# Kernel optimization log

Hardware: AMD Instinct MI355X
Metric: run time of the kernel (lower is better)

## Reference

```python
import jax, jax.numpy as jnp
import numpy as np

N_HEADS = 32
N_KV_HEADS = 8


def _rope_tables(T, half_dim):
    # standard rotary angle tables: theta_i = 10000^(-2i/D)
    inv_freq = 1.0 / (10000.0 ** (np.arange(half_dim, dtype=np.float32) / half_dim))
    ang = np.arange(T, dtype=np.float32)[:, None] * inv_freq[None, :]  # [T, D/2]
    return jnp.asarray(np.sin(ang)), jnp.asarray(np.cos(ang))


def setup_inputs() -> dict:
    key = jax.random.key(0)
    ks = jax.random.split(key, 5)
    B, T, C = 1, 2048, 2048
    hd = C // N_HEADS  # 64
    kv_dim = N_KV_HEADS * hd  # 512
    w_scale = 0.02
    x = jax.random.normal(ks[0], (B, T, C), dtype=jnp.float32)
    Wq = jax.random.normal(ks[1], (C, C), dtype=jnp.float32) * w_scale
    Wk = jax.random.normal(ks[2], (C, kv_dim), dtype=jnp.float32) * w_scale
    Wv = jax.random.normal(ks[3], (C, kv_dim), dtype=jnp.float32) * w_scale
    Wo = jax.random.normal(ks[4], (C, C), dtype=jnp.float32) * w_scale
    rope_sin, rope_cos = _rope_tables(T, hd // 2)
    return {"x": x, "Wq": Wq, "Wk": Wk, "Wv": Wv, "Wo": Wo,
            "rope_sin": rope_sin, "rope_cos": rope_cos, "swa_window": 1024}


def apply_rope(x, sin, cos):
    # x: [B, T, H, D]; sin/cos: [T, D/2]; interleaved-pair rotation
    B, T, H, D = x.shape
    xr = x.reshape(B, T, H, D // 2, 2)
    x1, x2 = xr[..., 0], xr[..., 1]
    s = sin[None, :, None, :]
    c = cos[None, :, None, :]
    o1 = x1 * c - x2 * s
    o2 = x1 * s + x2 * c
    return jnp.stack((o1, o2), axis=-1).reshape(B, T, H, D)


def reference(x, Wq, Wk, Wv, Wo, rope_sin, rope_cos, swa_window):
    B, T, C = x.shape
    hd = C // N_HEADS
    g = N_HEADS // N_KV_HEADS
    q = (x @ Wq).reshape(B, T, N_HEADS, hd)
    k = (x @ Wk).reshape(B, T, N_KV_HEADS, hd)
    v = (x @ Wv).reshape(B, T, N_KV_HEADS, hd)
    q = apply_rope(q, rope_sin, rope_cos)
    k = apply_rope(k, rope_sin, rope_cos)
    # GQA: expand kv heads (repeat_interleave along head dim)
    k = jnp.repeat(k, g, axis=2)
    v = jnp.repeat(v, g, axis=2)
    q = q.transpose(0, 2, 1, 3)  # [B, H, T, D]
    k = k.transpose(0, 2, 1, 3)
    v = v.transpose(0, 2, 1, 3)
    scores = jnp.einsum('bhqd,bhkd->bhqk', q, k) / jnp.sqrt(jnp.float32(hd))
    idx = jnp.arange(T)
    rel = idx[:, None] - idx[None, :]  # query_pos - key_pos
    # masked-out: future tokens (rel < 0) or older than the sliding window
    masked = (rel < 0) | (rel > swa_window)
    scores = jnp.where(masked[None, None], jnp.float32(-1e30), scores)
    attn = jax.nn.softmax(scores, axis=-1)
    out = jnp.einsum('bhqk,bhkd->bhqd', attn, v)
    out = out.transpose(0, 2, 1, 3).reshape(B, T, C)
    return out @ Wo
```

## Files before the change

kernel.cpp:

```cpp
#include <hip/hip_runtime.h>

typedef __attribute__((ext_vector_type(8))) short short8;
typedef __attribute__((ext_vector_type(4))) float f32x4;
typedef unsigned short u16;

#define T_SEQ 2048
#define C_DIM 2048
#define QKV_N 3072
#define HD 64


static __device__ __forceinline__ u16 f2bf(float f) {
    unsigned u = __builtin_bit_cast(unsigned, f);
    unsigned rounding = 0x7fffu + ((u >> 16) & 1u);
    return (u16)((u + rounding) >> 16);
}

static __device__ __forceinline__ void gld_lds16(void* lds, const void* g) {
    __builtin_amdgcn_global_load_lds(
        (const __attribute__((address_space(1))) unsigned int*)g,
        (__attribute__((address_space(3))) unsigned int*)lds, 16, 0, 0);
}


__global__ __launch_bounds__(256) void convert_bf16_k(const float* __restrict__ in,
                                                      u16* __restrict__ out) {
    int i = (blockIdx.x * 256 + threadIdx.x) * 4;
    f32x4 v = *(const f32x4*)(in + i);
    u16* o = out + i;
    o[0] = f2bf(v[0]); o[1] = f2bf(v[1]); o[2] = f2bf(v[2]); o[3] = f2bf(v[3]);
}


__global__ __launch_bounds__(256) void transpose_conv(const float* __restrict__ W,
                                                      u16* __restrict__ Wt,
                                                      int N, int row_off) {
    __shared__ float tile[32][33];
    int n0 = blockIdx.x * 32, k0 = blockIdx.y * 32;
    int tx = threadIdx.x & 31, ty = threadIdx.x >> 5;
#pragma unroll
    for (int i = 0; i < 4; i++)
        tile[ty + i * 8][tx] = W[(size_t)(k0 + ty + i * 8) * N + n0 + tx];
    __syncthreads();
#pragma unroll
    for (int i = 0; i < 4; i++)
        Wt[(size_t)(row_off + n0 + ty + i * 8) * 2048 + k0 + tx] = f2bf(tile[tx][ty + i * 8]);
}


__global__ __launch_bounds__(256) void gemm_bt(const u16* __restrict__ A,
                                               const u16* __restrict__ BT,
                                               float* __restrict__ C,
                                               int M, int N, int K) {
    __shared__ alignas(16) u16 As[128][32];
    __shared__ alignas(16) u16 Bs[128][32];
    const int m0 = blockIdx.x * 128;
    const int n0 = blockIdx.y * 128;
    const int w = threadIdx.x >> 6, lane = threadIdx.x & 63;
    const int lo = lane & 15, hi = lane >> 4;
    const int wr = w >> 1, wc = w & 1;

    f32x4 zero4 = {0.f, 0.f, 0.f, 0.f};
    f32x4 acc[4][4];
#pragma unroll
    for (int m = 0; m < 4; m++)
#pragma unroll
        for (int n = 0; n < 4; n++) acc[m][n] = zero4;

    for (int k0 = 0; k0 < K; k0 += 32) {
#pragma unroll
        for (int i = 0; i < 2; i++) {
            int c = (w * 2 + i) * 64 + lane;
            int row = c >> 2, cc = (c & 3) * 8;
            gld_lds16((char*)&As[0][0] + (w * 2 + i) * 1024,
                      A + (size_t)(m0 + row) * K + k0 + cc);
            gld_lds16((char*)&Bs[0][0] + (w * 2 + i) * 1024,
                      BT + (size_t)(n0 + row) * K + k0 + cc);
        }
        __syncthreads();
        short8 a[4], b[4];
#pragma unroll
        for (int m = 0; m < 4; m++) a[m] = *(const short8*)&As[wr * 64 + m * 16 + lo][hi * 8];
#pragma unroll
        for (int n = 0; n < 4; n++) b[n] = *(const short8*)&Bs[wc * 64 + n * 16 + lo][hi * 8];
#pragma unroll
        for (int m = 0; m < 4; m++)
#pragma unroll
            for (int n = 0; n < 4; n++)
                acc[m][n] = __builtin_amdgcn_mfma_f32_16x16x32_bf16(a[m], b[n], acc[m][n], 0, 0, 0);
        __syncthreads();
    }
#pragma unroll
    for (int m = 0; m < 4; m++)
#pragma unroll
        for (int n = 0; n < 4; n++) {
            int col = n0 + wc * 64 + n * 16 + lo;
#pragma unroll
            for (int r = 0; r < 4; r++) {
                int row = m0 + wr * 64 + m * 16 + hi * 4 + r;
                C[(size_t)row * N + col] = acc[m][n][r];
            }
        }
}


__global__ __launch_bounds__(256) void rope_conv(const float* __restrict__ qkv,
                                                 const float* __restrict__ sn,
                                                 const float* __restrict__ cs,
                                                 u16* __restrict__ qb,
                                                 u16* __restrict__ kb,
                                                 u16* __restrict__ vt) {
    int t = blockIdx.x / 6;
    int idx = (blockIdx.x % 6) * 256 + threadIdx.x;
    const float* row = qkv + (size_t)t * QKV_N;
    if (idx < 1024) {
        int h = idx >> 5, pr = idx & 31;
        float x1 = row[h * 64 + 2 * pr], x2 = row[h * 64 + 2 * pr + 1];
        float s = sn[t * 32 + pr], c = cs[t * 32 + pr];
        float o1 = (x1 * c - x2 * s) * 0.125f;
        float o2 = (x1 * s + x2 * c) * 0.125f;
        unsigned pack = (unsigned)f2bf(o1) | ((unsigned)f2bf(o2) << 16);
        *(unsigned*)(qb + (size_t)t * C_DIM + h * 64 + 2 * pr) = pack;
    } else if (idx < 1280) {
        int j = idx - 1024;
        int kh = j >> 5, pr = j & 31;
        float x1 = row[2048 + kh * 64 + 2 * pr], x2 = row[2048 + kh * 64 + 2 * pr + 1];
        float s = sn[t * 32 + pr], c = cs[t * 32 + pr];
        float o1 = x1 * c - x2 * s;
        float o2 = x1 * s + x2 * c;
        unsigned pack = (unsigned)f2bf(o1) | ((unsigned)f2bf(o2) << 16);
        *(unsigned*)(kb + ((size_t)kh * T_SEQ + t) * 64 + 2 * pr) = pack;
    } else {
        int j = idx - 1280;
        int kh = j >> 5, dl = (j & 31) * 2;
        float v0 = row[2560 + kh * 64 + dl], v1 = row[2560 + kh * 64 + dl + 1];
        vt[((size_t)kh * 64 + dl) * T_SEQ + t] = f2bf(v0);
        vt[((size_t)kh * 64 + dl + 1) * T_SEQ + t] = f2bf(v1);
    }
}


__global__ __launch_bounds__(256) void attn_fwd(const u16* __restrict__ qb,
                                                const u16* __restrict__ kb,
                                                const u16* __restrict__ vt,
                                                u16* __restrict__ ob,
                                                const int* __restrict__ winp) {
    __shared__ alignas(16) char KsB[8192];
    __shared__ alignas(16) char VsB[8192];
    __shared__ alignas(16) u16 Ps[4][16][88];
    const int window = *winp;
    const int h = blockIdx.y, kvh = h >> 2;
    const int q0 = blockIdx.x * 64;
    const int w = threadIdx.x >> 6, lane = threadIdx.x & 63;
    const int lo = lane & 15, hi = lane >> 4;

    const int qrow = q0 + w * 16 + lo;
    const short8 qa0 = *(const short8*)(qb + (size_t)qrow * C_DIM + h * HD + hi * 8);
    const short8 qa1 = *(const short8*)(qb + (size_t)qrow * C_DIM + h * HD + 32 + hi * 8);

    f32x4 zero4 = {0.f, 0.f, 0.f, 0.f};
    f32x4 acc[4];
#pragma unroll
    for (int dt = 0; dt < 4; dt++) acc[dt] = zero4;
    float lreg[4] = {0.f, 0.f, 0.f, 0.f};

    int kt0 = q0 - window; if (kt0 < 0) kt0 = 0; kt0 &= ~63;
    const int qlo_w = q0 + w * 16, qhi_w = qlo_w + 15;

    for (int kt = kt0; kt < q0 + 64; kt += 64) {
#pragma unroll
        for (int j = 0; j < 2; j++) {
            int c = (w * 2 + j) * 64 + lane;
            int rr = c >> 3, sc = (c & 7) ^ (rr & 7);
            gld_lds16(KsB + (w * 2 + j) * 1024,
                      kb + ((size_t)kvh * T_SEQ + kt + rr) * 64 + sc * 8);
            gld_lds16(VsB + (w * 2 + j) * 1024,
                      vt + ((size_t)kvh * 64 + rr) * T_SEQ + kt + sc * 8);
        }
        __syncthreads();
        if (kt <= qhi_w && kt + 63 >= qlo_w - window) {
            const bool interior = (kt + 63 <= qlo_w) && (qhi_w - kt <= window);
            f32x4 s0, s1, s2, s3;
            {
#define QK_TILE(SD, NT)                                                              \
                {                                                                    \
                    int key = (NT) * 16 + lo;                                        \
                    const short8 kf0 = *(const short8*)(KsB + key * 128 + ((hi ^ (key & 7)) << 4));       \
                    const short8 kf1 = *(const short8*)(KsB + key * 128 + (((4 + hi) ^ (key & 7)) << 4)); \
                    f32x4 z = zero4;                                                 \
                    z = __builtin_amdgcn_mfma_f32_16x16x32_bf16(qa0, kf0, z, 0, 0, 0);\
                    z = __builtin_amdgcn_mfma_f32_16x16x32_bf16(qa1, kf1, z, 0, 0, 0);\
                    SD = z;                                                          \
                }
                QK_TILE(s0, 0) QK_TILE(s1, 1) QK_TILE(s2, 2) QK_TILE(s3, 3)
#undef QK_TILE
            }
            if (!interior) {
#define MASK_TILE(SD, NT)                                                            \
                {                                                                    \
                    int key = kt + (NT) * 16 + lo;                                   \
                    _Pragma("unroll")                                                \
                    for (int r = 0; r < 4; r++) {                                    \
                        int q = qlo_w + hi * 4 + r;                                  \
                        if ((unsigned)(q - key) > (unsigned)window) SD[r] = -1e30f;  \
                    }                                                                \
                }
                MASK_TILE(s0, 0) MASK_TILE(s1, 1) MASK_TILE(s2, 2) MASK_TILE(s3, 3)
#undef MASK_TILE
            }
#define EXP_TILE(SD, NT)                                                             \
            {                                                                        \
                _Pragma("unroll")                                                    \
                for (int r = 0; r < 4; r++) {                                        \
                    float p = __expf(SD[r]);                                         \
                    lreg[r] += p;                                                    \
                    Ps[w][hi * 4 + r][(NT) * 16 + lo] = f2bf(p);                     \
                }                                                                    \
            }
            EXP_TILE(s0, 0) EXP_TILE(s1, 1) EXP_TILE(s2, 2) EXP_TILE(s3, 3)
#undef EXP_TILE
            const short8 pa0 = *(const short8*)&Ps[w][lo][hi * 8];
            const short8 pa1 = *(const short8*)&Ps[w][lo][32 + hi * 8];
#pragma unroll
            for (int dt = 0; dt < 4; dt++) {
                int d = dt * 16 + lo;
                const short8 vf0 = *(const short8*)(VsB + d * 128 + ((hi ^ (d & 7)) << 4));
                const short8 vf1 = *(const short8*)(VsB + d * 128 + (((4 + hi) ^ (d & 7)) << 4));
                acc[dt] = __builtin_amdgcn_mfma_f32_16x16x32_bf16(pa0, vf0, acc[dt], 0, 0, 0);
                acc[dt] = __builtin_amdgcn_mfma_f32_16x16x32_bf16(pa1, vf1, acc[dt], 0, 0, 0);
            }
        }
        __syncthreads();
    }
    float inv[4];
#pragma unroll
    for (int r = 0; r < 4; r++) {
        float l = lreg[r];
        l += __shfl_xor(l, 1);
        l += __shfl_xor(l, 2);
        l += __shfl_xor(l, 4);
        l += __shfl_xor(l, 8);
        inv[r] = 1.0f / l;
    }
#pragma unroll
    for (int dt = 0; dt < 4; dt++)
#pragma unroll
        for (int r = 0; r < 4; r++) {
            int q = qlo_w + hi * 4 + r;
            ob[(size_t)q * C_DIM + h * HD + dt * 16 + lo] = f2bf(acc[dt][r] * inv[r]);
        }
}


extern "C" void kernel_launch(void* const* d_in, const int* in_sizes, int n_in,
                              void* d_out, int out_size, void* d_ws, size_t ws_size,
                              hipStream_t stream) {
    const float* x  = (const float*)d_in[0];
    const float* Wq = (const float*)d_in[1];
    const float* Wk = (const float*)d_in[2];
    const float* Wv = (const float*)d_in[3];
    const float* Wo = (const float*)d_in[4];
    const float* rs = (const float*)d_in[5];
    const float* rc = (const float*)d_in[6];
    const int*  win = (const int*)d_in[7];
    float* out = (float*)d_out;

    char* w = (char*)d_ws;
    u16*   xb   = (u16*)(w);
    u16*   Wt   = (u16*)(w + (8ull  << 20));
    u16*   Wot  = (u16*)(w + (20ull << 20));
    float* qkv  = (float*)(w + (28ull << 20));
    u16*   qb   = (u16*)(w + (52ull << 20));
    u16*   kbuf = (u16*)(w + (60ull << 20));
    u16*   vtb  = (u16*)(w + (62ull << 20));
    u16*   attb = (u16*)(w + (64ull << 20));

    convert_bf16_k<<<4096, 256, 0, stream>>>(x, xb);
    transpose_conv<<<dim3(64, 64), 256, 0, stream>>>(Wq, Wt, 2048, 0);
    transpose_conv<<<dim3(16, 64), 256, 0, stream>>>(Wk, Wt, 512, 2048);
    transpose_conv<<<dim3(16, 64), 256, 0, stream>>>(Wv, Wt, 512, 2560);
    transpose_conv<<<dim3(64, 64), 256, 0, stream>>>(Wo, Wot, 2048, 0);
    gemm_bt<<<dim3(16, 24), 256, 0, stream>>>(xb, Wt, qkv, 2048, 3072, 2048);
    rope_conv<<<2048 * 6, 256, 0, stream>>>(qkv, rs, rc, qb, kbuf, vtb);
    attn_fwd<<<dim3(32, 32), 256, 0, stream>>>(qb, kbuf, vtb, attb, win);
    gemm_bt<<<dim3(16, 16), 256, 0, stream>>>(attb, Wot, out, 2048, 2048, 2048);
}
```

Before: 267.1 us.

## Double-buffer GEMM and attention LDS tiles, widen GEMM K-step, merge weight transposes

The GEMM now stages 64-wide K tiles into two XOR-swizzled LDS buffers and prefetches the next tile while running MFMAs on the current one. This halves the number of barriers per K and hides global-load latency. The attention kernel gets the same double-buffered K/V staging. The four weight transpose launches are merged into one kernel. The cost is doubled LDS use, which may reduce occupancy, and relying on a single barrier per iteration to order prefetches against reads.

```diff
diff --git a/kernel.cpp b/kernel.cpp
--- a/kernel.cpp
+++ b/kernel.cpp
@@ -32,11 +32,20 @@
 }
 
 
-__global__ __launch_bounds__(256) void transpose_conv(const float* __restrict__ W,
-                                                      u16* __restrict__ Wt,
-                                                      int N, int row_off) {
+__global__ __launch_bounds__(256) void transpose_all(const float* __restrict__ Wq,
+                                                     const float* __restrict__ Wk,
+                                                     const float* __restrict__ Wv,
+                                                     const float* __restrict__ Wo,
+                                                     u16* __restrict__ Wt,
+                                                     u16* __restrict__ Wot) {
     __shared__ float tile[32][33];
-    int n0 = blockIdx.x * 32, k0 = blockIdx.y * 32;
+    int bx = blockIdx.x;
+    const float* W; u16* D; int N, row_off;
+    if (bx < 64)      { W = Wq; D = Wt;  N = 2048; row_off = 0;    }
+    else if (bx < 80) { W = Wk; D = Wt;  N = 512;  row_off = 2048; bx -= 64; }
+    else if (bx < 96) { W = Wv; D = Wt;  N = 512;  row_off = 2560; bx -= 80; }
+    else              { W = Wo; D = Wot; N = 2048; row_off = 0;    bx -= 96; }
+    int n0 = bx * 32, k0 = blockIdx.y * 32;
     int tx = threadIdx.x & 31, ty = threadIdx.x >> 5;
 #pragma unroll
     for (int i = 0; i < 4; i++)
@@ -44,7 +53,7 @@
     __syncthreads();
 #pragma unroll
     for (int i = 0; i < 4; i++)
-        Wt[(size_t)(row_off + n0 + ty + i * 8) * 2048 + k0 + tx] = f2bf(tile[tx][ty + i * 8]);
+        D[(size_t)(row_off + n0 + ty + i * 8) * 2048 + k0 + tx] = f2bf(tile[tx][ty + i * 8]);
 }
 
 
@@ -52,13 +61,14 @@
                                                const u16* __restrict__ BT,
                                                float* __restrict__ C,
                                                int M, int N, int K) {
-    __shared__ alignas(16) u16 As[128][32];
-    __shared__ alignas(16) u16 Bs[128][32];
+    __shared__ alignas(16) u16 As[2][128][64];
+    __shared__ alignas(16) u16 Bs[2][128][64];
     const int m0 = blockIdx.x * 128;
     const int n0 = blockIdx.y * 128;
     const int w = threadIdx.x >> 6, lane = threadIdx.x & 63;
     const int lo = lane & 15, hi = lane >> 4;
     const int wr = w >> 1, wc = w & 1;
+    const int srcsw = ((lane & 7) ^ (lane >> 3)) * 8;
 
     f32x4 zero4 = {0.f, 0.f, 0.f, 0.f};
     f32x4 acc[4][4];
@@ -67,27 +77,42 @@
 #pragma unroll
         for (int n = 0; n < 4; n++) acc[m][n] = zero4;
 
-    for (int k0 = 0; k0 < K; k0 += 32) {
-#pragma unroll
-        for (int i = 0; i < 2; i++) {
-            int c = (w * 2 + i) * 64 + lane;
-            int row = c >> 2, cc = (c & 3) * 8;
-            gld_lds16((char*)&As[0][0] + (w * 2 + i) * 1024,
-                      A + (size_t)(m0 + row) * K + k0 + cc);
-            gld_lds16((char*)&Bs[0][0] + (w * 2 + i) * 1024,
-                      BT + (size_t)(n0 + row) * K + k0 + cc);
-        }
-        __syncthreads();
-        short8 a[4], b[4];
-#pragma unroll
-        for (int m = 0; m < 4; m++) a[m] = *(const short8*)&As[wr * 64 + m * 16 + lo][hi * 8];
-#pragma unroll
-        for (int n = 0; n < 4; n++) b[n] = *(const short8*)&Bs[wc * 64 + n * 16 + lo][hi * 8];
-#pragma unroll
-        for (int m = 0; m < 4; m++)
-#pragma unroll
-            for (int n = 0; n < 4; n++)
-                acc[m][n] = __builtin_amdgcn_mfma_f32_16x16x32_bf16(a[m], b[n], acc[m][n], 0, 0, 0);
+    auto stage = [&](int buf, int k0) {
+#pragma unroll
+        for (int j = 0; j < 4; j++) {
+            int row = (w * 4 + j) * 8 + (lane >> 3);
+            gld_lds16((char*)&As[buf][0][0] + (w * 4 + j) * 1024,
+                      A + (size_t)(m0 + row) * K + k0 + srcsw);
+            gld_lds16((char*)&Bs[buf][0][0] + (w * 4 + j) * 1024,
+                      BT + (size_t)(n0 + row) * K + k0 + srcsw);
+        }
+    };
+
+    stage(0, 0);
+    __syncthreads();
+    const int nk = K >> 6;
+    for (int t = 0; t < nk; t++) {
+        const int cur = t & 1;
+        if (t + 1 < nk) stage(cur ^ 1, (t + 1) * 64);
+#pragma unroll
+        for (int kk = 0; kk < 2; kk++) {
+            short8 a[4], b[4];
+#pragma unroll
+            for (int m = 0; m < 4; m++) {
+                int r = wr * 64 + m * 16 + lo;
+                a[m] = *(const short8*)((const char*)&As[cur][0][0] + r * 128 + (((kk * 4 + hi) ^ (lo & 7)) << 4));
+            }
+#pragma unroll
+            for (int n = 0; n < 4; n++) {
+                int r = wc * 64 + n * 16 + lo;
+                b[n] = *(const short8*)((const char*)&Bs[cur][0][0] + r * 128 + (((kk * 4 + hi) ^ (lo & 7)) << 4));
+            }
+#pragma unroll
+            for (int m = 0; m < 4; m++)
+#pragma unroll
+                for (int n = 0; n < 4; n++)
+                    acc[m][n] = __builtin_amdgcn_mfma_f32_16x16x32_bf16(a[m], b[n], acc[m][n], 0, 0, 0);
+        }
         __syncthreads();
     }
 #pragma unroll
@@ -145,8 +170,8 @@
                                                 const u16* __restrict__ vt,
                                                 u16* __restrict__ ob,
                                                 const int* __restrict__ winp) {
-    __shared__ alignas(16) char KsB[8192];
-    __shared__ alignas(16) char VsB[8192];
+    __shared__ alignas(16) char KsB[2][8192];
+    __shared__ alignas(16) char VsB[2][8192];
     __shared__ alignas(16) u16 Ps[4][16][88];
     const int window = *winp;
     const int h = blockIdx.y, kvh = h >> 2;
@@ -166,18 +191,26 @@
 
     int kt0 = q0 - window; if (kt0 < 0) kt0 = 0; kt0 &= ~63;
     const int qlo_w = q0 + w * 16, qhi_w = qlo_w + 15;
-
-    for (int kt = kt0; kt < q0 + 64; kt += 64) {
+    const int nt = (q0 + 64 - kt0) >> 6;
+
+    auto stage = [&](int buf, int kt) {
 #pragma unroll
         for (int j = 0; j < 2; j++) {
             int c = (w * 2 + j) * 64 + lane;
             int rr = c >> 3, sc = (c & 7) ^ (rr & 7);
-            gld_lds16(KsB + (w * 2 + j) * 1024,
+            gld_lds16(KsB[buf] + (w * 2 + j) * 1024,
                       kb + ((size_t)kvh * T_SEQ + kt + rr) * 64 + sc * 8);
-            gld_lds16(VsB + (w * 2 + j) * 1024,
+            gld_lds16(VsB[buf] + (w * 2 + j) * 1024,
                       vt + ((size_t)kvh * 64 + rr) * T_SEQ + kt + sc * 8);
         }
-        __syncthreads();
+    };
+
+    stage(0, kt0);
+    __syncthreads();
+    for (int i = 0; i < nt; i++) {
+        const int kt = kt0 + i * 64;
+        const int cur = i & 1;
+        if (i + 1 < nt) stage(cur ^ 1, kt + 64);
         if (kt <= qhi_w && kt + 63 >= qlo_w - window) {
             const bool interior = (kt + 63 <= qlo_w) && (qhi_w - kt <= window);
             f32x4 s0, s1, s2, s3;
@@ -185,8 +218,8 @@
 #define QK_TILE(SD, NT)                                                              \
                 {                                                                    \
                     int key = (NT) * 16 + lo;                                        \
-                    const short8 kf0 = *(const short8*)(KsB + key * 128 + ((hi ^ (key & 7)) << 4));       \
-                    const short8 kf1 = *(const short8*)(KsB + key * 128 + (((4 + hi) ^ (key & 7)) << 4)); \
+                    const short8 kf0 = *(const short8*)(KsB[cur] + key * 128 + ((hi ^ (key & 7)) << 4));       \
+                    const short8 kf1 = *(const short8*)(KsB[cur] + key * 128 + (((4 + hi) ^ (key & 7)) << 4)); \
                     f32x4 z = zero4;                                                 \
                     z = __builtin_amdgcn_mfma_f32_16x16x32_bf16(qa0, kf0, z, 0, 0, 0);\
                     z = __builtin_amdgcn_mfma_f32_16x16x32_bf16(qa1, kf1, z, 0, 0, 0);\
@@ -224,8 +257,8 @@
 #pragma unroll
             for (int dt = 0; dt < 4; dt++) {
                 int d = dt * 16 + lo;
-                const short8 vf0 = *(const short8*)(VsB + d * 128 + ((hi ^ (d & 7)) << 4));
-                const short8 vf1 = *(const short8*)(VsB + d * 128 + (((4 + hi) ^ (d & 7)) << 4));
+                const short8 vf0 = *(const short8*)(VsB[cur] + d * 128 + ((hi ^ (d & 7)) << 4));
+                const short8 vf1 = *(const short8*)(VsB[cur] + d * 128 + (((4 + hi) ^ (d & 7)) << 4));
                 acc[dt] = __builtin_amdgcn_mfma_f32_16x16x32_bf16(pa0, vf0, acc[dt], 0, 0, 0);
                 acc[dt] = __builtin_amdgcn_mfma_f32_16x16x32_bf16(pa1, vf1, acc[dt], 0, 0, 0);
             }
@@ -276,10 +309,7 @@
     u16*   attb = (u16*)(w + (64ull << 20));
 
     convert_bf16_k<<<4096, 256, 0, stream>>>(x, xb);
-    transpose_conv<<<dim3(64, 64), 256, 0, stream>>>(Wq, Wt, 2048, 0);
-    transpose_conv<<<dim3(16, 64), 256, 0, stream>>>(Wk, Wt, 512, 2048);
-    transpose_conv<<<dim3(16, 64), 256, 0, stream>>>(Wv, Wt, 512, 2560);
-    transpose_conv<<<dim3(64, 64), 256, 0, stream>>>(Wo, Wot, 2048, 0);
+    transpose_all<<<dim3(160, 64), 256, 0, stream>>>(Wq, Wk, Wv, Wo, Wt, Wot);
     gemm_bt<<<dim3(16, 24), 256, 0, stream>>>(xb, Wt, qkv, 2048, 3072, 2048);
     rope_conv<<<2048 * 6, 256, 0, stream>>>(qkv, rs, rc, qb, kbuf, vtb);
     attn_fwd<<<dim3(32, 32), 256, 0, stream>>>(qb, kbuf, vtb, attb, win);
```

New measurement: 248.4 us. 7.0% less time.
